# Kernel tuning notes

Measured on AMD Instinct MI355X. Metric: run time of the kernel, lower is better.

The kernel has to match this reference:

```python
import jax, jax.numpy as jnp
import numpy as np

DIM_IN = 10000
LW = [512, 512]
EW = [16, 16]


def setup_inputs() -> dict:
    key = jax.random.key(0)
    ks = jax.random.split(key, 16)
    x = jax.random.normal(ks[0], (4096, DIM_IN), dtype=jnp.float32)
    mask = jax.random.randint(ks[1], (4096, DIM_IN), 0, 2).astype(jnp.float32)
    s = 0.02
    # LNet: dim_in -> 512 -> 512 -> dim_in (tanh after hidden layers only)
    W1 = jax.random.normal(ks[2], (DIM_IN, LW[0]), dtype=jnp.float32) * s
    b1 = jnp.zeros((LW[0],), jnp.float32)
    W2 = jax.random.normal(ks[3], (LW[0], LW[1]), dtype=jnp.float32) * s
    b2 = jnp.zeros((LW[1],), jnp.float32)
    W3 = jax.random.normal(ks[4], (LW[1], DIM_IN), dtype=jnp.float32) * s
    b3 = jnp.zeros((DIM_IN,), jnp.float32)
    # ENet: 1 -> 16 -> 16 -> 1
    E1w = jax.random.normal(ks[5], (1, EW[0]), dtype=jnp.float32) * s
    E1b = jnp.zeros((EW[0],), jnp.float32)
    E2w = jax.random.normal(ks[6], (EW[0], EW[1]), dtype=jnp.float32) * s
    E2b = jnp.zeros((EW[1],), jnp.float32)
    E3w = jax.random.normal(ks[7], (EW[1], 1), dtype=jnp.float32) * s
    E3b = jnp.zeros((1,), jnp.float32)
    return {"x": x, "mask": mask, "W1": W1, "b1": b1, "W2": W2, "b2": b2,
            "W3": W3, "b3": b3, "E1w": E1w, "E1b": E1b, "E2w": E2w,
            "E2b": E2b, "E3w": E3w, "E3b": E3b}


def reference(x, mask, W1, b1, W2, b2, W3, b3, E1w, E1b, E2w, E2b, E3w, E3b):
    # LNet: two tanh hidden layers + final linear
    h = jnp.tanh(x @ W1 + b1)            # [B, 512]
    h = jnp.tanh(h @ W2 + b2)            # [B, 512]
    out = h @ W3 + b3                    # [B, dim_in]
    # ENet applied elementwise to scalar entries; original gathers x[mask>0],
    # runs ENet, adds 0.8*y residual, scatters back. Equivalent dense form:
    v = out[..., None]                   # [B, dim_in, 1]
    e = jnp.tanh(v @ E1w + E1b)          # [B, dim_in, 16]
    e = jnp.tanh(e @ E2w + E2b)          # [B, dim_in, 16]
    e = (e @ E3w + E3b)[..., 0]          # [B, dim_in]
    y = e + 0.8 * out
    return jnp.where(mask > 0, y, out)
```

## Files before the change

kernel.cpp:

```cpp
#include <hip/hip_runtime.h>
#include <stdint.h>

typedef unsigned short u16;
typedef u16 u16x8 __attribute__((ext_vector_type(8)));
typedef __bf16 bf16x8 __attribute__((ext_vector_type(8)));
typedef float f32x4 __attribute__((ext_vector_type(4)));

__device__ __forceinline__ float b2f(u16 u) {
    union { unsigned int i; float f; } c; c.i = ((unsigned int)u) << 16; return c.f;
}
__device__ __forceinline__ u16 f2b(float f) {
    unsigned int u = __float_as_uint(f);
    u += 0x7fff + ((u >> 16) & 1);
    return (u16)(u >> 16);
}

__global__ __launch_bounds__(1024) void detect_dtype(const u16* __restrict__ m,
                                                     int* __restrict__ flag) {
    __shared__ int s;
    int t = threadIdx.x;
    if (t == 0) s = 0;
    __syncthreads();
    if (m[2 * t] != 0) atomicOr(&s, 1);
    __syncthreads();
    if (t == 0) *flag = s;
}

template<int DT>
__global__ __launch_bounds__(256) void canon_params(
        const void* b1, const void* b2, const void* b3,
        const void* E1w, const void* E1b, const void* E2w,
        const void* E2b, const void* E3w, const void* E3b,
        const int* __restrict__ flag, float* __restrict__ dst) {
    if (*flag != DT) return;
    int i = blockIdx.x * 256 + threadIdx.x;
    if (i >= 11345) return;
    const void* srcs[9] = {b1, b2, b3, E1w, E1b, E2w, E2b, E3w, E3b};
    const int off[10] = {0, 512, 1024, 11024, 11040, 11056, 11312, 11328, 11344, 11345};
    int s = 0;
    while (i >= off[s + 1]) ++s;
    int j = i - off[s];
    dst[i] = (DT == 1) ? b2f(((const u16*)srcs[s])[j]) : ((const float*)srcs[s])[j];
}

template<int DT>
__global__ __launch_bounds__(256) void transpose_pad(const void* __restrict__ vin,
        u16* __restrict__ out, const int* __restrict__ flag,
        int R, int C, int ldi, int ldo) {
    if (*flag != DT) return;
    __shared__ __align__(16) u16 tile[64][72];
    const int rt = blockIdx.x * 64;
    const int ct = blockIdx.y * 64;
    const int t = threadIdx.x;
    const int lr = t >> 2;
    const int lc = (t & 3) * 16;
    const int r = rt + lr;
    if (r < R && (ct + lc + 15) < C) {
        if (DT == 1) {
            const u16* p = (const u16*)vin + (long)r * ldi + ct + lc;
            *(u16x8*)&tile[lr][lc]     = *(const u16x8*)p;
            *(u16x8*)&tile[lr][lc + 8] = *(const u16x8*)(p + 8);
        } else {
            const float* p = (const float*)vin + (long)r * ldi + ct + lc;
            #pragma unroll
            for (int q = 0; q < 4; ++q) {
                f32x4 v4 = *(const f32x4*)(p + q * 4);
                #pragma unroll
                for (int j = 0; j < 4; ++j) tile[lr][lc + q * 4 + j] = f2b(v4[j]);
            }
        }
    } else {
        #pragma unroll
        for (int j = 0; j < 16; ++j) {
            int c = ct + lc + j;
            u16 v = 0;
            if (r < R && c < C)
                v = (DT == 1) ? ((const u16*)vin)[(long)r * ldi + c]
                              : f2b(((const float*)vin)[(long)r * ldi + c]);
            tile[lr][lc + j] = v;
        }
    }
    __syncthreads();
    const int oc = ct + lr;
    if (oc >= C) return;
    u16x8 w0, w1;
    #pragma unroll
    for (int j = 0; j < 8; ++j) w0[j] = tile[lc + j][lr];
    #pragma unroll
    for (int j = 0; j < 8; ++j) w1[j] = tile[lc + 8 + j][lr];
    long ob = (long)oc * ldo + rt + lc;
    if (rt + lc + 15 < ldo) {
        *(u16x8*)(out + ob)     = w0;
        *(u16x8*)(out + ob + 8) = w1;
    } else {
        #pragma unroll
        for (int j = 0; j < 16; ++j) {
            int orr = rt + lc + j;
            if (orr < ldo) out[(long)oc * ldo + orr] = (j < 8) ? w0[j] : w1[j - 8];
        }
    }
}

__global__ __launch_bounds__(256) void build_elut(const float* __restrict__ P,
                                                  float* __restrict__ lut) {
    const float* E1w = P + 11024; const float* E1b = P + 11040;
    const float* E2w = P + 11056; const float* E2b = P + 11312;
    const float* E3w = P + 11328; const float* E3b = P + 11344;
    int i = blockIdx.x * 256 + threadIdx.x;
    if (i >= 4096) return;
    float v = -16.f + (float)i * (1.f / 128.f);
    float e1[16];
    #pragma unroll
    for (int j = 0; j < 16; ++j) e1[j] = tanhf(v * E1w[j] + E1b[j]);
    float e = E3b[0];
    #pragma unroll
    for (int k = 0; k < 16; ++k) {
        float s = E2b[k];
        #pragma unroll
        for (int j = 0; j < 16; ++j) s += e1[j] * E2w[j * 16 + k];
        e += tanhf(s) * E3w[k];
    }
    lut[i] = e;
}

template<int MODE, int XDT>
__global__ __launch_bounds__(256, 2) void gemm_bt(
        const void* __restrict__ A, const u16* __restrict__ Bt,
        const float* __restrict__ biasf, void* __restrict__ Cb,
        float* __restrict__ Cf, const void* __restrict__ mask,
        const float* __restrict__ lut, const int* __restrict__ flag,
        int M, int N, int K, int Kloop, int kchunk, int ldA, int ldB, int ldC) {
    if (flag && *flag != XDT) return;
    constexpr int ADT = (MODE == 2) ? XDT : 1;

    __shared__ __align__(16) u16 Alds[128 * 32];
    __shared__ __align__(16) u16 Blds[128 * 32];
    __shared__ __align__(16) float lutS[(MODE == 1) ? 4096 : 4];

    const int tid = threadIdx.x;
    const int m0 = blockIdx.x * 128;
    const int n0 = blockIdx.y * 128;
    const int lane = tid & 63;
    const int w = tid >> 6;
    const int wm = (w >> 1) * 64;
    const int wn = (w & 1) * 64;
    const int lm = lane & 15;
    const int lq = lane >> 4;

    if (MODE == 1) {
        const f32x4* s = (const f32x4*)lut;
        f32x4* d = (f32x4*)lutS;
        #pragma unroll
        for (int i = 0; i < 4; ++i) d[tid + 256 * i] = s[tid + 256 * i];
    }

    const int arow = tid >> 2;
    const int kq8 = (tid & 3) * 8;
    const long aoff = (long)(m0 + arow) * ldA + kq8;
    const long boff = (long)(n0 + arow) * ldB + kq8;
    u16* aldst0 = &Alds[tid * 8];
    u16* aldst1 = &Alds[tid * 8 + 2048];
    u16* bldst0 = &Blds[tid * 8];
    u16* bldst1 = &Blds[tid * 8 + 2048];
    const bool bv0 = (n0 + arow) < N;
    const bool bv1 = (n0 + arow + 64) < N;

    const u16* aB = &Alds[(wm + lm) * 32 + lq * 8];
    const u16* bB = &Blds[(wn + lm) * 32 + lq * 8];

    const f32x4 zero = {0.f, 0.f, 0.f, 0.f};
    const u16x8 z8 = {0, 0, 0, 0, 0, 0, 0, 0};
    f32x4 acc[4][4];
    #pragma unroll
    for (int i = 0; i < 4; ++i)
        #pragma unroll
        for (int j = 0; j < 4; ++j) acc[i][j] = zero;

    int kb = 0, ke = Kloop;
    if (MODE == 2) { kb = blockIdx.z * kchunk; ke = min(Kloop, kb + kchunk); }

    for (int k0 = kb; k0 < ke; k0 += 32) {
        const bool av = (k0 + kq8) < K;
        u16x8 ra0 = z8, ra1 = z8;
        if (ADT == 1) {
            const u16* Au = (const u16*)A;
            if (av) {
                ra0 = *(const u16x8*)(Au + aoff + k0);
                ra1 = *(const u16x8*)(Au + aoff + 64 * (long)ldA + k0);
            }
        } else {
            const float* Af = (const float*)A;
            if (av) {
                f32x4 l0 = *(const f32x4*)(Af + aoff + k0);
                f32x4 h0 = *(const f32x4*)(Af + aoff + k0 + 4);
                f32x4 l1 = *(const f32x4*)(Af + aoff + 64 * (long)ldA + k0);
                f32x4 h1 = *(const f32x4*)(Af + aoff + 64 * (long)ldA + k0 + 4);
                #pragma unroll
                for (int j = 0; j < 4; ++j) {
                    ra0[j] = f2b(l0[j]); ra0[4 + j] = f2b(h0[j]);
                    ra1[j] = f2b(l1[j]); ra1[4 + j] = f2b(h1[j]);
                }
            }
        }
        u16x8 rb0 = bv0 ? *(const u16x8*)(Bt + boff + k0) : z8;
        u16x8 rb1 = bv1 ? *(const u16x8*)(Bt + boff + 64 * (long)ldB + k0) : z8;
        __syncthreads();
        *(u16x8*)aldst0 = ra0;
        *(u16x8*)aldst1 = ra1;
        *(u16x8*)bldst0 = rb0;
        *(u16x8*)bldst1 = rb1;
        __syncthreads();
        bf16x8 a[4], b[4];
        #pragma unroll
        for (int i = 0; i < 4; ++i) a[i] = *(const bf16x8*)(aB + i * 512);
        #pragma unroll
        for (int i = 0; i < 4; ++i) b[i] = *(const bf16x8*)(bB + i * 512);
        #pragma unroll
        for (int mi = 0; mi < 4; ++mi)
            #pragma unroll
            for (int ni = 0; ni < 4; ++ni)
                acc[mi][ni] = __builtin_amdgcn_mfma_f32_16x16x32_bf16(
                    a[mi], b[ni], acc[mi][ni], 0, 0, 0);
    }

    if (MODE == 2) {
        float* dst = Cf + (long)blockIdx.z * M * (long)N;
        #pragma unroll
        for (int mi = 0; mi < 4; ++mi) {
            const int row0 = m0 + wm + mi * 16 + lq * 4;
            #pragma unroll
            for (int ni = 0; ni < 4; ++ni) {
                const int col = n0 + wn + ni * 16 + lm;
                #pragma unroll
                for (int r = 0; r < 4; ++r)
                    dst[(long)(row0 + r) * ldC + col] = acc[mi][ni][r];
            }
        }
    } else if (MODE == 0) {
        #pragma unroll
        for (int mi = 0; mi < 4; ++mi) {
            const int row0 = m0 + wm + mi * 16 + lq * 4;
            #pragma unroll
            for (int ni = 0; ni < 4; ++ni) {
                const int col = n0 + wn + ni * 16 + lm;
                const float bc = biasf[col];
                #pragma unroll
                for (int r = 0; r < 4; ++r) {
                    float v = acc[mi][ni][r] + bc;
                    ((u16*)Cb)[(long)(row0 + r) * ldC + col] = f2b(tanhf(v));
                }
            }
        }
    } else {
        #pragma unroll
        for (int mi = 0; mi < 4; ++mi) {
            const int row0 = m0 + wm + mi * 16 + lq * 4;
            #pragma unroll
            for (int ni = 0; ni < 4; ++ni) {
                const int col = n0 + wn + ni * 16 + lm;
                if (col < N) {
                    const float bc = biasf[col];
                    #pragma unroll
                    for (int r = 0; r < 4; ++r) {
                        float v = acc[mi][ni][r] + bc;
                        float fi = (v + 16.f) * 128.f + 0.5f;
                        int idx = (int)fi;
                        idx = idx < 0 ? 0 : (idx > 4095 ? 4095 : idx);
                        float y = lutS[idx] + 0.8f * v;
                        long off = (long)(row0 + r) * ldC + col;
                        float mk = (XDT == 1) ? b2f(((const u16*)mask)[off])
                                              : ((const float*)mask)[off];
                        float res = mk > 0.f ? y : v;
                        if (XDT == 1) ((u16*)Cb)[off] = f2b(res);
                        else          ((float*)Cb)[off] = res;
                    }
                }
            }
        }
    }
}

__global__ __launch_bounds__(256) void reduce_tanh4(const float* __restrict__ p,
        const float* __restrict__ biasf, u16* __restrict__ h, int MN) {
    int i = (blockIdx.x * 256 + threadIdx.x) * 4;
    if (i >= MN) return;
    f32x4 s = *(const f32x4*)(p + i);
    s += *(const f32x4*)(p + (long)MN + i);
    s += *(const f32x4*)(p + 2L * MN + i);
    s += *(const f32x4*)(p + 3L * MN + i);
    int col = i & 511;
    #pragma unroll
    for (int c = 0; c < 4; ++c)
        h[i + c] = f2b(tanhf(s[c] + biasf[col + c]));
}

extern "C" void kernel_launch(void* const* d_in, const int* in_sizes, int n_in,
                              void* d_out, int out_size, void* d_ws, size_t ws_size,
                              hipStream_t stream) {
    const void* x    = d_in[0];
    const void* mask = d_in[1];
    const void* W1   = d_in[2];
    const void* b1   = d_in[3];
    const void* W2   = d_in[4];
    const void* b2   = d_in[5];
    const void* W3   = d_in[6];
    const void* b3   = d_in[7];

    const int B = 4096, D = 10000, H = 512, KP = 10016;

    char* ob = (char*)d_out;
    u16*   W1T     = (u16*)ob;
    float* partial = (float*)(ob + 10256384);
    u16*   h1      = (u16*)(ob + 43810816);
    u16*   W2T     = (u16*)(ob + 48005120);

    char* ws = (char*)d_ws;
    u16*   W3T   = (u16*)ws;
    u16*   h2    = (u16*)(ws + 10240000);
    float* elut  = (float*)(ws + 14434304);
    int*   flag  = (int*)(ws + 14450688);
    float* canon = (float*)(ws + 14450704);
    float* b1f = canon, * b2f = canon + 512, * b3f = canon + 1024;

    detect_dtype<<<1, 1024, 0, stream>>>((const u16*)mask, flag);

    canon_params<0><<<45, 256, 0, stream>>>(b1, b2, b3, d_in[8], d_in[9],
        d_in[10], d_in[11], d_in[12], d_in[13], flag, canon);
    canon_params<1><<<45, 256, 0, stream>>>(b1, b2, b3, d_in[8], d_in[9],
        d_in[10], d_in[11], d_in[12], d_in[13], flag, canon);

    transpose_pad<0><<<dim3(157, 8), 256, 0, stream>>>(W1, W1T, flag, D, H, H, KP);
    transpose_pad<1><<<dim3(157, 8), 256, 0, stream>>>(W1, W1T, flag, D, H, H, KP);
    transpose_pad<0><<<dim3(8, 8),   256, 0, stream>>>(W2, W2T, flag, H, H, H, H);
    transpose_pad<1><<<dim3(8, 8),   256, 0, stream>>>(W2, W2T, flag, H, H, H, H);
    transpose_pad<0><<<dim3(8, 157), 256, 0, stream>>>(W3, W3T, flag, H, D, D, H);
    transpose_pad<1><<<dim3(8, 157), 256, 0, stream>>>(W3, W3T, flag, H, D, D, H);

    build_elut<<<16, 256, 0, stream>>>(canon, elut);

    gemm_bt<2, 0><<<dim3(32, 4, 4), 256, 0, stream>>>(x, W1T, nullptr, nullptr,
        partial, nullptr, nullptr, flag, B, H, D, KP, 2528, D, KP, H);
    gemm_bt<2, 1><<<dim3(32, 4, 4), 256, 0, stream>>>(x, W1T, nullptr, nullptr,
        partial, nullptr, nullptr, flag, B, H, D, KP, 2528, D, KP, H);
    reduce_tanh4<<<(B * H) / 1024, 256, 0, stream>>>(partial, b1f, h1, B * H);

    gemm_bt<0, 1><<<dim3(32, 4), 256, 0, stream>>>(h1, W2T, b2f, h2, nullptr,
        nullptr, nullptr, nullptr, B, H, H, H, 0, H, H, H);

    gemm_bt<1, 0><<<dim3(32, 79), 256, 0, stream>>>(h2, W3T, b3f, d_out, nullptr,
        mask, elut, flag, B, D, H, H, 0, H, H, D);
    gemm_bt<1, 1><<<dim3(32, 79), 256, 0, stream>>>(h2, W3T, b3f, d_out, nullptr,
        mask, elut, flag, B, D, H, H, 0, H, H, D);
}
```

Before: 658.7 us.

## Use direct global-to-LDS loads with XOR swizzle, deeper split-K, runtime dtype dispatch

For bf16 A operands, the GEMM now loads tiles straight into LDS with global_load_lds instead of staging them in registers. A matching XOR swizzle on the LDS column index is meant to avoid bank conflicts. Split-K for the first layer goes from 4 to 8 chunks to raise occupancy, and launch bounds now allow 4 blocks per CU. The dual-template canon/transpose launches become a single kernel that branches on the runtime flag, and scratch buffers are moved so the extra partials fit. The trade-off is more partial-sum memory traffic in the reduce, and register pressure under the tighter launch bound.

After: 624.9 us. 5.1% less time.

```diff
diff --git a/kernel.cpp b/kernel.cpp
--- a/kernel.cpp
+++ b/kernel.cpp
@@ -13,6 +13,12 @@
     unsigned int u = __float_as_uint(f);
     u += 0x7fff + ((u >> 16) & 1);
     return (u16)(u >> 16);
+}
+
+typedef const __attribute__((address_space(1))) unsigned int* gas_p;
+typedef __attribute__((address_space(3))) unsigned int* las_p;
+__device__ __forceinline__ void gll16(const void* g, void* l) {
+    __builtin_amdgcn_global_load_lds((gas_p)g, (las_p)l, 16, 0, 0);
 }
 
 __global__ __launch_bounds__(1024) void detect_dtype(const u16* __restrict__ m,
@@ -26,13 +32,12 @@
     if (t == 0) *flag = s;
 }
 
-template<int DT>
 __global__ __launch_bounds__(256) void canon_params(
         const void* b1, const void* b2, const void* b3,
         const void* E1w, const void* E1b, const void* E2w,
         const void* E2b, const void* E3w, const void* E3b,
         const int* __restrict__ flag, float* __restrict__ dst) {
-    if (*flag != DT) return;
+    const int DT = *flag;
     int i = blockIdx.x * 256 + threadIdx.x;
     if (i >= 11345) return;
     const void* srcs[9] = {b1, b2, b3, E1w, E1b, E2w, E2b, E3w, E3b};
@@ -43,11 +48,10 @@
     dst[i] = (DT == 1) ? b2f(((const u16*)srcs[s])[j]) : ((const float*)srcs[s])[j];
 }
 
-template<int DT>
 __global__ __launch_bounds__(256) void transpose_pad(const void* __restrict__ vin,
         u16* __restrict__ out, const int* __restrict__ flag,
         int R, int C, int ldi, int ldo) {
-    if (*flag != DT) return;
+    const int DT = *flag;
     __shared__ __align__(16) u16 tile[64][72];
     const int rt = blockIdx.x * 64;
     const int ct = blockIdx.y * 64;
@@ -124,7 +128,7 @@
 }
 
 template<int MODE, int XDT>
-__global__ __launch_bounds__(256, 2) void gemm_bt(
+__global__ __launch_bounds__(256, 4) void gemm_bt(
         const void* __restrict__ A, const u16* __restrict__ Bt,
         const float* __restrict__ biasf, void* __restrict__ Cb,
         float* __restrict__ Cf, const void* __restrict__ mask,
@@ -132,6 +136,7 @@
         int M, int N, int K, int Kloop, int kchunk, int ldA, int ldB, int ldC) {
     if (flag && *flag != XDT) return;
     constexpr int ADT = (MODE == 2) ? XDT : 1;
+    constexpr bool GLL = (ADT == 1);
 
     __shared__ __align__(16) u16 Alds[128 * 32];
     __shared__ __align__(16) u16 Blds[128 * 32];
@@ -155,7 +160,7 @@
     }
 
     const int arow = tid >> 2;
-    const int kq8 = (tid & 3) * 8;
+    const int kq8 = (((tid & 3) ^ (arow & 3))) * 8;
     const long aoff = (long)(m0 + arow) * ldA + kq8;
     const long boff = (long)(n0 + arow) * ldB + kq8;
     u16* aldst0 = &Alds[tid * 8];
@@ -165,8 +170,9 @@
     const bool bv0 = (n0 + arow) < N;
     const bool bv1 = (n0 + arow + 64) < N;
 
-    const u16* aB = &Alds[(wm + lm) * 32 + lq * 8];
-    const u16* bB = &Blds[(wn + lm) * 32 + lq * 8];
+    const int sx = (lq ^ (lm & 3)) * 8;
+    const u16* aB = &Alds[(wm + lm) * 32 + sx];
+    const u16* bB = &Blds[(wn + lm) * 32 + sx];
 
     const f32x4 zero = {0.f, 0.f, 0.f, 0.f};
     const u16x8 z8 = {0, 0, 0, 0, 0, 0, 0, 0};
@@ -179,37 +185,47 @@
     int kb = 0, ke = Kloop;
     if (MODE == 2) { kb = blockIdx.z * kchunk; ke = min(Kloop, kb + kchunk); }
 
+    const u16* Au16 = (const u16*)A;
+
     for (int k0 = kb; k0 < ke; k0 += 32) {
-        const bool av = (k0 + kq8) < K;
-        u16x8 ra0 = z8, ra1 = z8;
-        if (ADT == 1) {
-            const u16* Au = (const u16*)A;
-            if (av) {
-                ra0 = *(const u16x8*)(Au + aoff + k0);
-                ra1 = *(const u16x8*)(Au + aoff + 64 * (long)ldA + k0);
-            }
+        if (GLL && (k0 + 32 <= K)) {
+            __syncthreads();
+            gll16(Au16 + aoff + k0, aldst0);
+            gll16(Au16 + aoff + 64 * (long)ldA + k0, aldst1);
+            gll16(Bt + boff + k0, bldst0);
+            gll16(Bt + boff + 64 * (long)ldB + k0, bldst1);
+            __syncthreads();
         } else {
-            const float* Af = (const float*)A;
-            if (av) {
-                f32x4 l0 = *(const f32x4*)(Af + aoff + k0);
-                f32x4 h0 = *(const f32x4*)(Af + aoff + k0 + 4);
-                f32x4 l1 = *(const f32x4*)(Af + aoff + 64 * (long)ldA + k0);
-                f32x4 h1 = *(const f32x4*)(Af + aoff + 64 * (long)ldA + k0 + 4);
-                #pragma unroll
-                for (int j = 0; j < 4; ++j) {
-                    ra0[j] = f2b(l0[j]); ra0[4 + j] = f2b(h0[j]);
-                    ra1[j] = f2b(l1[j]); ra1[4 + j] = f2b(h1[j]);
+            const bool av = (k0 + kq8) < K;
+            u16x8 ra0 = z8, ra1 = z8;
+            if (ADT == 1) {
+                if (av) {
+                    ra0 = *(const u16x8*)(Au16 + aoff + k0);
+                    ra1 = *(const u16x8*)(Au16 + aoff + 64 * (long)ldA + k0);
                 }
-            }
-        }
-        u16x8 rb0 = bv0 ? *(const u16x8*)(Bt + boff + k0) : z8;
-        u16x8 rb1 = bv1 ? *(const u16x8*)(Bt + boff + 64 * (long)ldB + k0) : z8;
-        __syncthreads();
-        *(u16x8*)aldst0 = ra0;
-        *(u16x8*)aldst1 = ra1;
-        *(u16x8*)bldst0 = rb0;
-        *(u16x8*)bldst1 = rb1;
-        __syncthreads();
+            } else {
+                const float* Af = (const float*)A;
+                if (av) {
+                    f32x4 l0 = *(const f32x4*)(Af + aoff + k0);
+                    f32x4 h0 = *(const f32x4*)(Af + aoff + k0 + 4);
+                    f32x4 l1 = *(const f32x4*)(Af + aoff + 64 * (long)ldA + k0);
+                    f32x4 h1 = *(const f32x4*)(Af + aoff + 64 * (long)ldA + k0 + 4);
+                    #pragma unroll
+                    for (int j = 0; j < 4; ++j) {
+                        ra0[j] = f2b(l0[j]); ra0[4 + j] = f2b(h0[j]);
+                        ra1[j] = f2b(l1[j]); ra1[4 + j] = f2b(h1[j]);
+                    }
+                }
+            }
+            u16x8 rb0 = bv0 ? *(const u16x8*)(Bt + boff + k0) : z8;
+            u16x8 rb1 = bv1 ? *(const u16x8*)(Bt + boff + 64 * (long)ldB + k0) : z8;
+            __syncthreads();
+            *(u16x8*)aldst0 = ra0;
+            *(u16x8*)aldst1 = ra1;
+            *(u16x8*)bldst0 = rb0;
+            *(u16x8*)bldst1 = rb1;
+            __syncthreads();
+        }
         bf16x8 a[4], b[4];
         #pragma unroll
         for (int i = 0; i < 4; ++i) a[i] = *(const bf16x8*)(aB + i * 512);
@@ -280,14 +296,13 @@
     }
 }
 
-__global__ __launch_bounds__(256) void reduce_tanh4(const float* __restrict__ p,
+__global__ __launch_bounds__(256) void reduce_tanh8(const float* __restrict__ p,
         const float* __restrict__ biasf, u16* __restrict__ h, int MN) {
     int i = (blockIdx.x * 256 + threadIdx.x) * 4;
     if (i >= MN) return;
     f32x4 s = *(const f32x4*)(p + i);
-    s += *(const f32x4*)(p + (long)MN + i);
-    s += *(const f32x4*)(p + 2L * MN + i);
-    s += *(const f32x4*)(p + 3L * MN + i);
+    #pragma unroll
+    for (int z = 1; z < 8; ++z) s += *(const f32x4*)(p + (long)z * MN + i);
     int col = i & 511;
     #pragma unroll
     for (int c = 0; c < 4; ++c)
@@ -311,8 +326,8 @@
     char* ob = (char*)d_out;
     u16*   W1T     = (u16*)ob;
     float* partial = (float*)(ob + 10256384);
-    u16*   h1      = (u16*)(ob + 43810816);
-    u16*   W2T     = (u16*)(ob + 48005120);
+    u16*   h1      = (u16*)(ob + 77365248);
+    u16*   W2T     = (u16*)(ob + 10256384);
 
     char* ws = (char*)d_ws;
     u16*   W3T   = (u16*)ws;
@@ -324,25 +339,21 @@
 
     detect_dtype<<<1, 1024, 0, stream>>>((const u16*)mask, flag);
 
-    canon_params<0><<<45, 256, 0, stream>>>(b1, b2, b3, d_in[8], d_in[9],
+    canon_params<<<45, 256, 0, stream>>>(b1, b2, b3, d_in[8], d_in[9],
         d_in[10], d_in[11], d_in[12], d_in[13], flag, canon);
-    canon_params<1><<<45, 256, 0, stream>>>(b1, b2, b3, d_in[8], d_in[9],
-        d_in[10], d_in[11], d_in[12], d_in[13], flag, canon);
-
-    transpose_pad<0><<<dim3(157, 8), 256, 0, stream>>>(W1, W1T, flag, D, H, H, KP);
-    transpose_pad<1><<<dim3(157, 8), 256, 0, stream>>>(W1, W1T, flag, D, H, H, KP);
-    transpose_pad<0><<<dim3(8, 8),   256, 0, stream>>>(W2, W2T, flag, H, H, H, H);
-    transpose_pad<1><<<dim3(8, 8),   256, 0, stream>>>(W2, W2T, flag, H, H, H, H);
-    transpose_pad<0><<<dim3(8, 157), 256, 0, stream>>>(W3, W3T, flag, H, D, D, H);
-    transpose_pad<1><<<dim3(8, 157), 256, 0, stream>>>(W3, W3T, flag, H, D, D, H);
+
+    transpose_pad<<<dim3(157, 8), 256, 0, stream>>>(W1, W1T, flag, D, H, H, KP);
+    transpose_pad<<<dim3(8, 157), 256, 0, stream>>>(W3, W3T, flag, H, D, D, H);
 
     build_elut<<<16, 256, 0, stream>>>(canon, elut);
 
-    gemm_bt<2, 0><<<dim3(32, 4, 4), 256, 0, stream>>>(x, W1T, nullptr, nullptr,
-        partial, nullptr, nullptr, flag, B, H, D, KP, 2528, D, KP, H);
-    gemm_bt<2, 1><<<dim3(32, 4, 4), 256, 0, stream>>>(x, W1T, nullptr, nullptr,
-        partial, nullptr, nullptr, flag, B, H, D, KP, 2528, D, KP, H);
-    reduce_tanh4<<<(B * H) / 1024, 256, 0, stream>>>(partial, b1f, h1, B * H);
+    gemm_bt<2, 0><<<dim3(32, 4, 8), 256, 0, stream>>>(x, W1T, nullptr, nullptr,
+        partial, nullptr, nullptr, flag, B, H, D, KP, 1280, D, KP, H);
+    gemm_bt<2, 1><<<dim3(32, 4, 8), 256, 0, stream>>>(x, W1T, nullptr, nullptr,
+        partial, nullptr, nullptr, flag, B, H, D, KP, 1280, D, KP, H);
+    reduce_tanh8<<<(B * H) / 1024, 256, 0, stream>>>(partial, b1f, h1, B * H);
+
+    transpose_pad<<<dim3(8, 8), 256, 0, stream>>>(W2, W2T, flag, H, H, H, H);
 
     gemm_bt<0, 1><<<dim3(32, 4), 256, 0, stream>>>(h1, W2T, b2f, h2, nullptr,
         nullptr, nullptr, nullptr, B, H, H, H, 0, H, H, H);
```
